# Optimization experiments

Hardware: AMD Instinct MI355X
Metric: run time of the kernel (lower is better)

## Reference

```python
import jax, jax.numpy as jnp
import numpy as np

D_MODEL, D_STATE, D_CONV, EXPAND = 1024, 16, 4, 2
D_INNER = EXPAND * D_MODEL            # 2048
DT_RANK = D_MODEL // 16               # 64
B, L = 2, 4096


def setup_inputs() -> dict:
    key = jax.random.key(0)
    ks = jax.random.split(key, 8)
    s = 0.02
    u = jax.random.normal(ks[0], (B, L, D_MODEL), jnp.float32)
    in_proj_w = jax.random.normal(ks[1], (2 * D_INNER, D_MODEL), jnp.float32) * s
    conv_w = jax.random.normal(ks[2], (D_INNER, D_CONV), jnp.float32) * 0.2
    conv_b = jnp.zeros((D_INNER,), jnp.float32)
    x_proj_w = jax.random.normal(ks[3], (DT_RANK + 2 * D_STATE, D_INNER), jnp.float32) * s
    dt_proj_w = jax.random.normal(ks[4], (D_INNER, DT_RANK), jnp.float32) * (DT_RANK ** -0.5)
    # dt bias initialized so softplus(dt_bias) in [1e-3, 1e-1], as in mamba-ssm
    dt = jnp.exp(jax.random.uniform(ks[5], (D_INNER,)) * (np.log(0.1) - np.log(1e-3)) + np.log(1e-3))
    dt_bias = jnp.log(-jnp.expm1(-dt) * jnp.exp(dt))  # inverse softplus
    A_log = jnp.log(jnp.tile(jnp.arange(1, D_STATE + 1, dtype=jnp.float32), (D_INNER, 1)))
    D_in = jnp.ones((D_INNER,), jnp.float32)
    out_proj_w = jax.random.normal(ks[6], (D_MODEL, D_INNER), jnp.float32) * s
    D_skip = jnp.ones((D_MODEL,), jnp.float32)
    return dict(u=u, in_proj_w=in_proj_w, conv_w=conv_w, conv_b=conv_b,
                x_proj_w=x_proj_w, dt_proj_w=dt_proj_w, dt_bias=dt_bias,
                A_log=A_log, D_in=D_in, out_proj_w=out_proj_w, D_skip=D_skip)


def _mamba(u, in_proj_w, conv_w, conv_b, x_proj_w, dt_proj_w, dt_bias,
           A_log, D_in, out_proj_w):
    b, l, _ = u.shape
    xz = jnp.einsum('bld,ed->ble', u, in_proj_w)      # (B,L,2*Din)
    x, z = jnp.split(xz, 2, axis=-1)
    # causal depthwise conv1d over time, kernel size D_CONV
    xp = jnp.pad(x, ((0, 0), (D_CONV - 1, 0), (0, 0)))
    x = sum(xp[:, k:k + l, :] * conv_w[:, k] for k in range(D_CONV)) + conv_b
    x = jax.nn.silu(x)
    x_dbl = jnp.einsum('bld,ed->ble', x, x_proj_w)    # (B,L,dt_rank+2N)
    dt = jax.nn.softplus(x_dbl[..., :DT_RANK] @ dt_proj_w.T + dt_bias)  # (B,L,Din)
    Bm = x_dbl[..., DT_RANK:DT_RANK + D_STATE]        # (B,L,N)
    Cm = x_dbl[..., DT_RANK + D_STATE:]               # (B,L,N)
    A = -jnp.exp(A_log)                               # (Din,N)

    def step(h, inp):
        dt_t, B_t, C_t, x_t = inp                     # (B,Din),(B,N),(B,N),(B,Din)
        dA = jnp.exp(dt_t[..., None] * A)             # (B,Din,N)
        h = dA * h + (dt_t * x_t)[..., None] * B_t[:, None, :]
        y = jnp.einsum('bdn,bn->bd', h, C_t)
        return h, y

    h0 = jnp.zeros((b, D_INNER, D_STATE), u.dtype)
    xs = (dt.transpose(1, 0, 2), Bm.transpose(1, 0, 2),
          Cm.transpose(1, 0, 2), x.transpose(1, 0, 2))
    _, ys = jax.lax.scan(step, h0, xs)                # (L,B,Din)
    y = ys.transpose(1, 0, 2) + x * D_in
    y = y * jax.nn.silu(z)
    return jnp.einsum('bld,ed->ble', y, out_proj_w)   # (B,L,D_MODEL)


def reference(u, in_proj_w, conv_w, conv_b, x_proj_w, dt_proj_w, dt_bias,
              A_log, D_in, out_proj_w, D_skip):
    y = _mamba(u, in_proj_w, conv_w, conv_b, x_proj_w, dt_proj_w, dt_bias,
               A_log, D_in, out_proj_w)
    return y + D_skip[None, None, :] * u
```

## Files before the change

kernel.cpp:

```cpp
#include <hip/hip_runtime.h>

typedef unsigned short u16;
typedef unsigned int u32;
typedef __attribute__((ext_vector_type(8))) short s16x8;
typedef __attribute__((ext_vector_type(4))) float f32x4;

__device__ inline u16 f2bf(float f){
    u32 u = __float_as_uint(f);
    u32 r = (u + 0x7fffu + ((u >> 16) & 1u)) >> 16;
    return (u16)r;
}
__device__ inline float bf2f(u16 h){
    return __uint_as_float(((u32)h) << 16);
}

#define GLOAD_LDS16(g, l) __builtin_amdgcn_global_load_lds( \
    (__attribute__((address_space(1))) void*)(void*)(g),    \
    (__attribute__((address_space(3))) void*)(l), 16, 0, 0)

#define MEMFENCE asm volatile("" ::: "memory")

template<int EPI>
__global__ __launch_bounds__(512, 1) void gemm256(
    const u16* __restrict__ A, const u16* __restrict__ B,
    int M, int N, int K, int nbn,
    float* __restrict__ Cf, u16* __restrict__ Cb, u16* __restrict__ Cb2,
    const float* __restrict__ aux0, const float* __restrict__ aux1)
{
    __shared__ u16 lds[2][2][2][128 * 64];
    const int tid  = threadIdx.x;
    const int lane = tid & 63, wave = tid >> 6;
    const int wr = wave >> 2, wc = wave & 3;
    const int l16 = lane & 15, lg = lane >> 4;

    int wgid = blockIdx.x, nwg = gridDim.x;
    int swz = wgid;
    if ((nwg & 7) == 0) { int cpx = nwg >> 3; swz = (wgid & 7) * cpx + (wgid >> 3); }
    const int bm = swz / nbn, bn = swz % nbn;

    const u16* Ab = A + (size_t)bm * 256 * K;
    const u16* Bb = B + (size_t)bn * 256 * K;

    auto stage_half = [&](int kbuf, int mat, int half, int kt) {
        const u16* src = mat ? Bb : Ab;
        #pragma unroll
        for (int j = 0; j < 2; j++) {
            int slot = j * 512 + tid;
            int r = slot >> 3, cg = slot & 7;
            GLOAD_LDS16(src + (size_t)(half * 128 + r) * K + kt + ((cg ^ (r & 7)) << 3),
                        &lds[kbuf][mat][half][(j * 512 + wave * 64) * 8]);
        }
    };

    f32x4 acc[2][2][4][2] = {};
    s16x8 a[4][2], b0[2][2], b1[2][2];

    auto readA = [&](int kbuf, int mh) {
        #pragma unroll
        for (int m = 0; m < 4; m++)
            #pragma unroll
            for (int ks = 0; ks < 2; ks++) {
                int r = mh * 64 + m * 16 + l16;
                int cg = (ks * 4 + lg) ^ (l16 & 7);
                a[m][ks] = *(const s16x8*)&lds[kbuf][0][wr][r * 64 + cg * 8];
            }
    };
    auto readB = [&](int kbuf, int nh, s16x8 (&bb)[2][2]) {
        #pragma unroll
        for (int n = 0; n < 2; n++)
            #pragma unroll
            for (int ks = 0; ks < 2; ks++) {
                int row = wc * 64 + nh * 32 + n * 16 + l16;
                int half = row >> 7, r = row & 127;
                int cg = (ks * 4 + lg) ^ (l16 & 7);
                bb[n][ks] = *(const s16x8*)&lds[kbuf][1][half][r * 64 + cg * 8];
            }
    };

    auto phase_mfma = [&](int mh, int nh, s16x8 (&bb)[2][2]) {
        MEMFENCE;
        __builtin_amdgcn_s_barrier();
        asm volatile("s_waitcnt lgkmcnt(0)" ::: "memory");
        __builtin_amdgcn_sched_barrier(0);
        __builtin_amdgcn_s_setprio(1);
        #pragma unroll
        for (int m = 0; m < 4; m++)
            #pragma unroll
            for (int n = 0; n < 2; n++)
                #pragma unroll
                for (int ks = 0; ks < 2; ks++)
                    acc[mh][nh][m][n] = __builtin_amdgcn_mfma_f32_16x16x32_bf16(
                        a[m][ks], bb[n][ks], acc[mh][nh][m][n], 0, 0, 0);
        __builtin_amdgcn_s_setprio(0);
        MEMFENCE;
        __builtin_amdgcn_s_barrier();
        MEMFENCE;
    };

    const int NT = K >> 6;

    stage_half(0, 1, 0, 0); stage_half(0, 1, 1, 0);
    stage_half(0, 0, 0, 0); stage_half(0, 0, 1, 0);
    if (NT > 1) {
        stage_half(1, 1, 0, 64);
        stage_half(1, 0, 0, 64); stage_half(1, 0, 1, 64);
    }
    asm volatile("s_waitcnt vmcnt(6)" ::: "memory");
    MEMFENCE;
    __builtin_amdgcn_s_barrier();
    MEMFENCE;

    for (int it = 0; it < (NT >> 1); it++) {
        const int t1k = (2 * it + 1) << 6;
        const int t2k = (2 * it + 2) << 6;
        const int t3k = (2 * it + 3) << 6;
        const bool pre = (2 * it + 2) < NT;
        readA(0, 0); readB(0, 0, b0);
        stage_half(1, 1, 1, t1k);
        phase_mfma(0, 0, b0);
        readB(0, 1, b1);
        phase_mfma(0, 1, b1);
        readA(0, 1);
        if (pre) stage_half(0, 1, 0, t2k);
        phase_mfma(1, 1, b1);
        if (pre) stage_half(0, 1, 1, t2k);
        asm volatile("s_waitcnt vmcnt(4)" ::: "memory");
        phase_mfma(1, 0, b0);
        readA(1, 0); readB(1, 0, b0);
        if (pre) stage_half(0, 0, 0, t2k);
        phase_mfma(0, 0, b0);
        readB(1, 1, b1);
        if (pre) stage_half(0, 0, 1, t2k);
        phase_mfma(0, 1, b1);
        readA(1, 1);
        if (pre) stage_half(1, 1, 0, t3k);
        phase_mfma(1, 1, b1);
        if (pre) { stage_half(1, 0, 0, t3k); stage_half(1, 0, 1, t3k); }
        asm volatile("s_waitcnt vmcnt(6)" ::: "memory");
        phase_mfma(1, 0, b0);
    }

    #pragma unroll
    for (int mh = 0; mh < 2; mh++)
        #pragma unroll
        for (int nh = 0; nh < 2; nh++)
            #pragma unroll
            for (int m = 0; m < 4; m++)
                #pragma unroll
                for (int n = 0; n < 2; n++) {
                    const int col = bn * 256 + wc * 64 + nh * 32 + n * 16 + l16;
                    #pragma unroll
                    for (int r = 0; r < 4; r++) {
                        const int row = bm * 256 + wr * 128 + mh * 64 + m * 16 + lg * 4 + r;
                        float v = acc[mh][nh][m][n][r];
                        if (EPI == 0) {
                            if (col < 2048) Cb[(size_t)row * 2048 + col] = f2bf(v);
                            else            Cb2[(size_t)row * 2048 + (col - 2048)] = f2bf(v);
                        } else {
                            float o = v + aux0[col] * aux1[(size_t)row * N + col];
                            Cf[(size_t)row * N + col] = o;
                        }
                    }
                }
}

__global__ __launch_bounds__(256) void gemm_dt(
    const u16* __restrict__ A, const u16* __restrict__ B,
    int M, int N, int K,
    u16* __restrict__ Cb, const float* __restrict__ aux0)
{
    constexpr int BK = 64;
    __shared__ u16 As[128 * BK];
    __shared__ u16 Bs[128 * BK];
    const int tid  = threadIdx.x;
    const int lane = tid & 63, wave = tid >> 6;
    const int wr = wave >> 1, wc = wave & 1;
    const int bm = blockIdx.x, bn = blockIdx.y;
    const int l16 = lane & 15, lg = lane >> 4;

    const u16* Ab = A + (size_t)bm * 128 * K;
    const u16* Bb = B + (size_t)bn * 128 * K;

    f32x4 acc[4][4] = {};

    for (int kt = 0; kt < K; kt += BK) {
        #pragma unroll
        for (int p = 0; p < 4; p++) {
            int flat = (p * 256 + tid) * 8;
            int r = flat >> 6, c = flat & 63;
            GLOAD_LDS16(Ab + (size_t)r * K + kt + c, As + flat);
        }
        #pragma unroll
        for (int p = 0; p < 4; p++) {
            int flat = (p * 256 + tid) * 8;
            int r = flat >> 6, c = flat & 63;
            GLOAD_LDS16(Bb + (size_t)r * K + kt + c, Bs + flat);
        }
        asm volatile("s_waitcnt vmcnt(0)" ::: "memory");
        __syncthreads();
        #pragma unroll
        for (int kk = 0; kk < 2; kk++) {
            s16x8 a[4], b[4];
            #pragma unroll
            for (int m = 0; m < 4; m++)
                a[m] = *(const s16x8*)&As[(wr * 64 + m * 16 + l16) * BK + kk * 32 + lg * 8];
            #pragma unroll
            for (int n = 0; n < 4; n++)
                b[n] = *(const s16x8*)&Bs[(wc * 64 + n * 16 + l16) * BK + kk * 32 + lg * 8];
            #pragma unroll
            for (int m = 0; m < 4; m++)
                #pragma unroll
                for (int n = 0; n < 4; n++)
                    acc[m][n] = __builtin_amdgcn_mfma_f32_16x16x32_bf16(a[m], b[n], acc[m][n], 0, 0, 0);
        }
        __syncthreads();
    }

    const int row0 = bm * 128 + wr * 64 + lg * 4;
    const int col0 = bn * 128 + wc * 64 + l16;
    #pragma unroll
    for (int m = 0; m < 4; m++)
        #pragma unroll
        for (int n = 0; n < 4; n++) {
            const int col = col0 + n * 16;
            #pragma unroll
            for (int r = 0; r < 4; r++) {
                const int row = row0 + m * 16 + r;
                float t2 = acc[m][n][r] + aux0[col];
                float sp = (t2 > 15.f) ? t2 : __logf(1.f + __expf(t2));
                Cb[(size_t)row * N + col] = f2bf(sp);
            }
        }
}

__global__ __launch_bounds__(256) void gemm_xproj_sk(
    const u16* __restrict__ A, const u16* __restrict__ B,
    float* __restrict__ part)
{
    constexpr int BK = 64, K = 2048;
    __shared__ u16 As[128 * BK];
    __shared__ u16 Bs[128 * BK];
    const int tid  = threadIdx.x;
    const int lane = tid & 63, wave = tid >> 6;
    const int wr = wave >> 1, wc = wave & 1;
    const int bm = blockIdx.x, sk = blockIdx.y;
    const int l16 = lane & 15, lg = lane >> 4;

    const u16* Ab = A + (size_t)bm * 128 * K;
    const u16* Bb = B;
    const int kt0 = sk * 256;

    f32x4 acc[4][4] = {};

    for (int kt = kt0; kt < kt0 + 256; kt += BK) {
        #pragma unroll
        for (int p = 0; p < 4; p++) {
            int flat = (p * 256 + tid) * 8;
            int r = flat >> 6, c = flat & 63;
            GLOAD_LDS16(Ab + (size_t)r * K + kt + c, As + flat);
        }
        #pragma unroll
        for (int p = 0; p < 4; p++) {
            int flat = (p * 256 + tid) * 8;
            int r = flat >> 6, c = flat & 63;
            GLOAD_LDS16(Bb + (size_t)r * K + kt + c, Bs + flat);
        }
        asm volatile("s_waitcnt vmcnt(0)" ::: "memory");
        __syncthreads();
        #pragma unroll
        for (int kk = 0; kk < 2; kk++) {
            s16x8 a[4], b[4];
            #pragma unroll
            for (int m = 0; m < 4; m++)
                a[m] = *(const s16x8*)&As[(wr * 64 + m * 16 + l16) * BK + kk * 32 + lg * 8];
            #pragma unroll
            for (int n = 0; n < 4; n++)
                b[n] = *(const s16x8*)&Bs[(wc * 64 + n * 16 + l16) * BK + kk * 32 + lg * 8];
            #pragma unroll
            for (int m = 0; m < 4; m++)
                #pragma unroll
                for (int n = 0; n < 4; n++)
                    acc[m][n] = __builtin_amdgcn_mfma_f32_16x16x32_bf16(a[m], b[n], acc[m][n], 0, 0, 0);
        }
        __syncthreads();
    }

    float* pb = part + (size_t)sk * 8192 * 128;
    const int row0 = bm * 128 + wr * 64 + lg * 4;
    const int col0 = wc * 64 + l16;
    #pragma unroll
    for (int m = 0; m < 4; m++)
        #pragma unroll
        for (int n = 0; n < 4; n++)
            #pragma unroll
            for (int r = 0; r < 4; r++)
                pb[(size_t)(row0 + m * 16 + r) * 128 + col0 + n * 16] = acc[m][n][r];
}

__global__ __launch_bounds__(256) void combine_xproj(
    const float* __restrict__ part, u16* __restrict__ dtin,
    float* __restrict__ xBC)
{
    const int gid = blockIdx.x * 256 + threadIdx.x;
    const int row = gid >> 7, col = gid & 127;
    float s = 0.f;
    #pragma unroll
    for (int sk = 0; sk < 8; sk++) s += part[(size_t)sk * 8192 * 128 + gid];
    if (col < 64)      dtin[(size_t)row * 64 + col] = f2bf(s);
    else if (col < 96) xBC[(size_t)row * 32 + (col - 64)] = s;
}

__global__ __launch_bounds__(256) void cvt_all(
    const float* __restrict__ u, const float* __restrict__ Wi,
    const float* __restrict__ Wo, const float* __restrict__ Wdt,
    const float* __restrict__ Wx,
    u16* __restrict__ u_bf, u16* __restrict__ Wi_bf, u16* __restrict__ Wo_bf,
    u16* __restrict__ Wdt_bf, u16* __restrict__ Wx_bf)
{
    size_t i = ((size_t)blockIdx.x * 256 + threadIdx.x) * 4;
    const size_t E0 = 8388608, E1 = E0 + 4194304, E2 = E1 + 2097152, E3 = E2 + 131072;
    f32x4 v;
    u16* dst;
    size_t off;
    if (i < E0)      { off = i;      v = *(const f32x4*)(u + off);   dst = u_bf + off; }
    else if (i < E1) { off = i - E0; v = *(const f32x4*)(Wi + off);  dst = Wi_bf + off; }
    else if (i < E2) { off = i - E1; v = *(const f32x4*)(Wo + off);  dst = Wo_bf + off; }
    else if (i < E3) { off = i - E2; v = *(const f32x4*)(Wdt + off); dst = Wdt_bf + off; }
    else {
        off = i - E3;
        size_t row = off >> 11;
        if (row < 96) v = *(const f32x4*)(Wx + off);
        else          v = (f32x4){0.f, 0.f, 0.f, 0.f};
        dst = Wx_bf + off;
    }
    ushort4 o;
    o.x = f2bf(v[0]); o.y = f2bf(v[1]); o.z = f2bf(v[2]); o.w = f2bf(v[3]);
    *(ushort4*)dst = o;
}

__global__ __launch_bounds__(256) void conv_silu(
    const u16* __restrict__ xzx, const float* __restrict__ cw,
    const float* __restrict__ cb, u16* __restrict__ xc)
{
    const int tid = threadIdx.x;
    const int d0 = tid * 8;
    const int t0 = blockIdx.x * 16;
    const int b  = blockIdx.y;
    float W0[8], W1[8], W2[8], W3[8], BI[8];
    #pragma unroll
    for (int j = 0; j < 8; j++) {
        f32x4 w = *(const f32x4*)(cw + (size_t)(d0 + j) * 4);
        W0[j] = w[0]; W1[j] = w[1]; W2[j] = w[2]; W3[j] = w[3];
        BI[j] = cb[d0 + j];
    }
    const u16* xp = xzx + (size_t)(b * 4096) * 2048 + d0;
    u16* op = xc + (size_t)(b * 4096) * 2048 + d0;

    float x0[8], x1[8], x2[8];
    #pragma unroll
    for (int j = 0; j < 8; j++) { x0[j] = 0.f; x1[j] = 0.f; x2[j] = 0.f; }
    if (t0 >= 3) {
        s16x8 v0 = *(const s16x8*)(xp + (size_t)(t0 - 3) * 2048);
        s16x8 v1 = *(const s16x8*)(xp + (size_t)(t0 - 2) * 2048);
        s16x8 v2 = *(const s16x8*)(xp + (size_t)(t0 - 1) * 2048);
        #pragma unroll
        for (int j = 0; j < 8; j++) {
            x0[j] = bf2f((u16)v0[j]); x1[j] = bf2f((u16)v1[j]); x2[j] = bf2f((u16)v2[j]);
        }
    }
    #pragma unroll
    for (int k = 0; k < 16; k++) {
        int t = t0 + k;
        s16x8 cv = *(const s16x8*)(xp + (size_t)t * 2048);
        s16x8 o;
        #pragma unroll
        for (int j = 0; j < 8; j++) {
            float c = bf2f((u16)cv[j]);
            float s = BI[j] + W0[j] * x0[j] + W1[j] * x1[j] + W2[j] * x2[j] + W3[j] * c;
            float v = s * __fdividef(1.f, 1.f + __expf(-s));
            o[j] = (short)f2bf(v);
            x0[j] = x1[j]; x1[j] = x2[j]; x2[j] = c;
        }
        *(s16x8*)(op + (size_t)t * 2048) = o;
    }
}

__global__ __launch_bounds__(256) void scan_p1(
    const u16* __restrict__ dtb, const u16* __restrict__ xc,
    const float* __restrict__ xBC, const float* __restrict__ A_log,
    u16* __restrict__ Aagg, u16* __restrict__ Bagg)
{
    __shared__ float Bsh[64][16];
    const int tid = threadIdx.x;
    const int d = blockIdx.x * 256 + tid;
    const int c = blockIdx.y, b = blockIdx.z;

    {
        int ti = tid >> 2, p = tid & 3;
        f32x4 bv = *(const f32x4*)(xBC + ((size_t)(b * 4096 + c * 64 + ti)) * 32 + p * 4);
        *(f32x4*)&Bsh[ti][p * 4] = bv;
    }
    __syncthreads();

    float Adn[16];
    #pragma unroll
    for (int q = 0; q < 4; q++) {
        f32x4 al = *(const f32x4*)(A_log + (size_t)d * 16 + q * 4);
        #pragma unroll
        for (int j = 0; j < 4; j++) Adn[q * 4 + j] = -__expf(al[j]);
    }

    const size_t base = (size_t)(b * 4096 + c * 64) * 2048 + d;
    const u16* dtp = dtb + base;
    const u16* xp  = xc  + base;

    float h[16];
    #pragma unroll
    for (int n = 0; n < 16; n++) h[n] = 0.f;
    float sumdt = 0.f;

    float dtv = bf2f(dtp[0]), xv = bf2f(xp[0]);
    for (int t = 0; t < 64; t++) {
        float ndt = 0.f, nx = 0.f;
        if (t < 63) { ndt = bf2f(dtp[(size_t)(t + 1) * 2048]); nx = bf2f(xp[(size_t)(t + 1) * 2048]); }
        float dtx = dtv * xv;
        sumdt += dtv;
        f32x4 B0 = *(const f32x4*)&Bsh[t][0];
        f32x4 B1 = *(const f32x4*)&Bsh[t][4];
        f32x4 B2 = *(const f32x4*)&Bsh[t][8];
        f32x4 B3 = *(const f32x4*)&Bsh[t][12];
        #pragma unroll
        for (int n = 0; n < 16; n++) {
            float Bv = (n < 4) ? B0[n] : (n < 8) ? B1[n - 4] : (n < 12) ? B2[n - 8] : B3[n - 12];
            float aa = __expf(Adn[n] * dtv);
            h[n] = fmaf(aa, h[n], dtx * Bv);
        }
        dtv = ndt; xv = nx;
    }

    const size_t abase = ((size_t)(b * 2048 + d) * 16) * 64 + c;
    #pragma unroll
    for (int n = 0; n < 16; n++) {
        Aagg[abase + (size_t)n * 64] = f2bf(__expf(Adn[n] * sumdt));
        Bagg[abase + (size_t)n * 64] = f2bf(h[n]);
    }
}

__global__ __launch_bounds__(256) void scan_p2(
    const u16* __restrict__ Aagg, u16* __restrict__ BaggH0)
{
    const int gid = blockIdx.x * 256 + threadIdx.x;
    const size_t base = (size_t)gid * 64;
    s16x8 Ar[8], Br[8];
    #pragma unroll
    for (int i = 0; i < 8; i++) {
        Ar[i] = *(const s16x8*)(Aagg + base + i * 8);
        Br[i] = *(const s16x8*)(BaggH0 + base + i * 8);
    }
    s16x8 Hr[8];
    float h = 0.f;
    #pragma unroll
    for (int i = 0; i < 8; i++) {
        #pragma unroll
        for (int j = 0; j < 8; j++) {
            float ac = bf2f((u16)Ar[i][j]);
            float bc = bf2f((u16)Br[i][j]);
            Hr[i][j] = (short)f2bf(h);
            h = fmaf(ac, h, bc);
        }
    }
    #pragma unroll
    for (int i = 0; i < 8; i++)
        *(s16x8*)(BaggH0 + base + i * 8) = Hr[i];
}

__global__ __launch_bounds__(256) void scan_p3(
    const u16* __restrict__ dtb, const u16* __restrict__ xc,
    const float* __restrict__ xBC, const float* __restrict__ A_log,
    const u16* __restrict__ H0, const u16* __restrict__ xzz,
    const float* __restrict__ D_in, u16* __restrict__ yy)
{
    __shared__ float BCs[64][32];
    const int tid = threadIdx.x;
    const int d = blockIdx.x * 256 + tid;
    const int c = blockIdx.y, b = blockIdx.z;

    {
        int ti = tid >> 2, p = tid & 3;
        const float* src = xBC + ((size_t)(b * 4096 + c * 64 + ti)) * 32 + p * 8;
        f32x4 v0 = *(const f32x4*)src;
        f32x4 v1 = *(const f32x4*)(src + 4);
        *(f32x4*)&BCs[ti][p * 8] = v0;
        *(f32x4*)&BCs[ti][p * 8 + 4] = v1;
    }
    __syncthreads();

    float Adn[16];
    #pragma unroll
    for (int q = 0; q < 4; q++) {
        f32x4 al = *(const f32x4*)(A_log + (size_t)d * 16 + q * 4);
        #pragma unroll
        for (int j = 0; j < 4; j++) Adn[q * 4 + j] = -__expf(al[j]);
    }
    const float Dd = D_in[d];

    float h[16];
    const size_t hbase = ((size_t)(b * 2048 + d) * 16) * 64 + c;
    #pragma unroll
    for (int n = 0; n < 16; n++) h[n] = bf2f(H0[hbase + (size_t)n * 64]);

    const size_t base = (size_t)(b * 4096 + c * 64) * 2048 + d;
    const u16* dtp = dtb + base;
    const u16* xp  = xc  + base;
    const u16* zp  = xzz + base;
    u16* yp = yy + base;

    float dtv = bf2f(dtp[0]), xv = bf2f(xp[0]), zv = bf2f(zp[0]);
    for (int t = 0; t < 64; t++) {
        float ndt = 0.f, nx = 0.f, nz = 0.f;
        if (t < 63) {
            ndt = bf2f(dtp[(size_t)(t + 1) * 2048]);
            nx  = bf2f(xp[(size_t)(t + 1) * 2048]);
            nz  = bf2f(zp[(size_t)(t + 1) * 2048]);
        }
        float dtx = dtv * xv;
        f32x4 B0 = *(const f32x4*)&BCs[t][0];
        f32x4 B1 = *(const f32x4*)&BCs[t][4];
        f32x4 B2 = *(const f32x4*)&BCs[t][8];
        f32x4 B3 = *(const f32x4*)&BCs[t][12];
        f32x4 C0 = *(const f32x4*)&BCs[t][16];
        f32x4 C1 = *(const f32x4*)&BCs[t][20];
        f32x4 C2 = *(const f32x4*)&BCs[t][24];
        f32x4 C3 = *(const f32x4*)&BCs[t][28];
        float y = 0.f;
        #pragma unroll
        for (int n = 0; n < 16; n++) {
            float Bv = (n < 4) ? B0[n] : (n < 8) ? B1[n - 4] : (n < 12) ? B2[n - 8] : B3[n - 12];
            float Cv = (n < 4) ? C0[n] : (n < 8) ? C1[n - 4] : (n < 12) ? C2[n - 8] : C3[n - 12];
            float aa = __expf(Adn[n] * dtv);
            h[n] = fmaf(aa, h[n], dtx * Bv);
            y = fmaf(h[n], Cv, y);
        }
        float sz = zv * __fdividef(1.f, 1.f + __expf(-zv));
        float val = fmaf(xv, Dd, y) * sz;
        yp[(size_t)t * 2048] = f2bf(val);
        dtv = ndt; xv = nx; zv = nz;
    }
}

extern "C" void kernel_launch(void* const* d_in, const int* in_sizes, int n_in,
                              void* d_out, int out_size, void* d_ws, size_t ws_size,
                              hipStream_t stream)
{
    const float* u       = (const float*)d_in[0];
    const float* Wi      = (const float*)d_in[1];
    const float* conv_w  = (const float*)d_in[2];
    const float* conv_b  = (const float*)d_in[3];
    const float* Wx      = (const float*)d_in[4];
    const float* Wdt     = (const float*)d_in[5];
    const float* dt_bias = (const float*)d_in[6];
    const float* A_log   = (const float*)d_in[7];
    const float* D_in_   = (const float*)d_in[8];
    const float* Wo      = (const float*)d_in[9];
    const float* D_skip  = (const float*)d_in[10];
    float* out = (float*)d_out;
    (void)in_sizes; (void)n_in; (void)out_size;

    const size_t MB = 1u << 20;
    char* ws = (char*)d_ws;
    u16*   xzx    = (u16*)(ws + 0);
    float* xpart  = (float*)(ws + 0);
    u16*   Aagg   = (u16*)(ws + 0);
    u16*   BaggH0 = (u16*)(ws + 8 * MB);
    u16*   xzz    = (u16*)(ws + 32 * MB);
    u16*   xc     = (u16*)(ws + 64 * MB);
    u16*   u_bf   = (u16*)(ws + 96 * MB);
    u16*   Wi_bf  = (u16*)(ws + 112 * MB);
    u16*   dtb    = (u16*)(ws + 96 * MB);
    u16*   Wx_bf  = (u16*)(ws + 128 * MB);
    u16*   Wdt_bf = (u16*)(ws + 128 * MB + 512 * 1024);
    u16*   yybuf  = (u16*)(ws + 128 * MB);
    float* xBC    = (float*)(ws + 160 * MB);
    u16*   dtin   = (u16*)(ws + 161 * MB);
    u16*   Wo_bf  = (u16*)(ws + 162 * MB);
    const size_t NEED = 166 * MB;
    if (ws_size < NEED) return;

    cvt_all<<<14720, 256, 0, stream>>>(u, Wi, Wo, Wdt, Wx,
                                       u_bf, Wi_bf, Wo_bf, Wdt_bf, Wx_bf);

    gemm256<0><<<512, 512, 0, stream>>>(u_bf, Wi_bf, 8192, 4096, 1024, 16,
                                        nullptr, xzx, xzz, nullptr, nullptr);
    conv_silu<<<dim3(256, 2), 256, 0, stream>>>(xzx, conv_w, conv_b, xc);

    gemm_xproj_sk<<<dim3(64, 8), 256, 0, stream>>>(xc, Wx_bf, xpart);
    combine_xproj<<<4096, 256, 0, stream>>>(xpart, dtin, xBC);

    gemm_dt<<<dim3(64, 16), 256, 0, stream>>>(dtin, Wdt_bf, 8192, 2048, 64,
                                              dtb, dt_bias);

    scan_p1<<<dim3(8, 64, 2), 256, 0, stream>>>(dtb, xc, xBC, A_log, Aagg, BaggH0);
    scan_p2<<<256, 256, 0, stream>>>(Aagg, BaggH0);
    scan_p3<<<dim3(8, 64, 2), 256, 0, stream>>>(dtb, xc, xBC, A_log, BaggH0, xzz,
                                                D_in_, yybuf);

    gemm256<3><<<128, 512, 0, stream>>>(yybuf, Wo_bf, 8192, 1024, 2048, 4,
                                        out, nullptr, nullptr, D_skip, u);
}
```

Before: 383.4 us.

## Double-buffer GEMM fragment registers to overlap LDS reads with MFMA

The GEMM main loop now keeps separate register sets for A and B fragments (AX/AY, BX/BY, B1). The next phase's LDS reads are issued before the current phase's MFMAs, instead of waiting on lgkmcnt(0) before each MFMA block. This is meant to hide LDS read latency behind matrix work across the eight phases per iteration. The cost is higher VGPR pressure, and dropping the explicit waitcnt and sched_barrier leaves ordering to the compiler.

```diff
diff --git a/kernel.cpp b/kernel.cpp
--- a/kernel.cpp
+++ b/kernel.cpp
@@ -19,6 +19,7 @@
     (__attribute__((address_space(3))) void*)(l), 16, 0, 0)
 
 #define MEMFENCE asm volatile("" ::: "memory")
+#define BAR do { MEMFENCE; __builtin_amdgcn_s_barrier(); MEMFENCE; } while (0)
 
 template<int EPI>
 __global__ __launch_bounds__(512, 1) void gemm256(
@@ -53,19 +54,19 @@
     };
 
     f32x4 acc[2][2][4][2] = {};
-    s16x8 a[4][2], b0[2][2], b1[2][2];
-
-    auto readA = [&](int kbuf, int mh) {
+    s16x8 AX[4][2], AY[4][2], BX[2][2], BY[2][2], B1[2][2];
+
+    auto readA = [&](int kbuf, int mh, s16x8 (&dst)[4][2]) {
         #pragma unroll
         for (int m = 0; m < 4; m++)
             #pragma unroll
             for (int ks = 0; ks < 2; ks++) {
                 int r = mh * 64 + m * 16 + l16;
                 int cg = (ks * 4 + lg) ^ (l16 & 7);
-                a[m][ks] = *(const s16x8*)&lds[kbuf][0][wr][r * 64 + cg * 8];
+                dst[m][ks] = *(const s16x8*)&lds[kbuf][0][wr][r * 64 + cg * 8];
             }
     };
-    auto readB = [&](int kbuf, int nh, s16x8 (&bb)[2][2]) {
+    auto readB = [&](int kbuf, int nh, s16x8 (&dst)[2][2]) {
         #pragma unroll
         for (int n = 0; n < 2; n++)
             #pragma unroll
@@ -73,15 +74,10 @@
                 int row = wc * 64 + nh * 32 + n * 16 + l16;
                 int half = row >> 7, r = row & 127;
                 int cg = (ks * 4 + lg) ^ (l16 & 7);
-                bb[n][ks] = *(const s16x8*)&lds[kbuf][1][half][r * 64 + cg * 8];
+                dst[n][ks] = *(const s16x8*)&lds[kbuf][1][half][r * 64 + cg * 8];
             }
     };
-
-    auto phase_mfma = [&](int mh, int nh, s16x8 (&bb)[2][2]) {
-        MEMFENCE;
-        __builtin_amdgcn_s_barrier();
-        asm volatile("s_waitcnt lgkmcnt(0)" ::: "memory");
-        __builtin_amdgcn_sched_barrier(0);
+    auto mfma16 = [&](int mh, int nh, s16x8 (&aa)[4][2], s16x8 (&bb)[2][2]) {
         __builtin_amdgcn_s_setprio(1);
         #pragma unroll
         for (int m = 0; m < 4; m++)
@@ -90,54 +86,51 @@
                 #pragma unroll
                 for (int ks = 0; ks < 2; ks++)
                     acc[mh][nh][m][n] = __builtin_amdgcn_mfma_f32_16x16x32_bf16(
-                        a[m][ks], bb[n][ks], acc[mh][nh][m][n], 0, 0, 0);
+                        aa[m][ks], bb[n][ks], acc[mh][nh][m][n], 0, 0, 0);
         __builtin_amdgcn_s_setprio(0);
-        MEMFENCE;
-        __builtin_amdgcn_s_barrier();
-        MEMFENCE;
     };
 
     const int NT = K >> 6;
 
     stage_half(0, 1, 0, 0); stage_half(0, 1, 1, 0);
     stage_half(0, 0, 0, 0); stage_half(0, 0, 1, 0);
-    if (NT > 1) {
-        stage_half(1, 1, 0, 64);
-        stage_half(1, 0, 0, 64); stage_half(1, 0, 1, 64);
-    }
+    stage_half(1, 1, 0, 64);
+    stage_half(1, 0, 0, 64); stage_half(1, 0, 1, 64);
     asm volatile("s_waitcnt vmcnt(6)" ::: "memory");
-    MEMFENCE;
-    __builtin_amdgcn_s_barrier();
-    MEMFENCE;
+    BAR;
+    readA(0, 0, AX); readB(0, 0, BX);
 
     for (int it = 0; it < (NT >> 1); it++) {
         const int t1k = (2 * it + 1) << 6;
         const int t2k = (2 * it + 2) << 6;
         const int t3k = (2 * it + 3) << 6;
         const bool pre = (2 * it + 2) < NT;
-        readA(0, 0); readB(0, 0, b0);
         stage_half(1, 1, 1, t1k);
-        phase_mfma(0, 0, b0);
-        readB(0, 1, b1);
-        phase_mfma(0, 1, b1);
-        readA(0, 1);
+        BAR; readB(0, 1, B1); mfma16(0, 0, AX, BX); BAR;
+        BAR; readA(0, 1, AY); mfma16(0, 1, AX, B1); BAR;
         if (pre) stage_half(0, 1, 0, t2k);
-        phase_mfma(1, 1, b1);
-        if (pre) stage_half(0, 1, 1, t2k);
-        asm volatile("s_waitcnt vmcnt(4)" ::: "memory");
-        phase_mfma(1, 0, b0);
-        readA(1, 0); readB(1, 0, b0);
+        BAR; mfma16(1, 1, AY, B1); BAR;
+        if (pre) {
+            stage_half(0, 1, 1, t2k);
+            asm volatile("s_waitcnt vmcnt(4)" ::: "memory");
+        } else {
+            asm volatile("s_waitcnt vmcnt(0)" ::: "memory");
+        }
+        BAR; readA(1, 0, AX); readB(1, 0, BY); mfma16(1, 0, AY, BX); BAR;
         if (pre) stage_half(0, 0, 0, t2k);
-        phase_mfma(0, 0, b0);
-        readB(1, 1, b1);
+        BAR; readB(1, 1, B1); mfma16(0, 0, AX, BY); BAR;
         if (pre) stage_half(0, 0, 1, t2k);
-        phase_mfma(0, 1, b1);
-        readA(1, 1);
+        BAR; readA(1, 1, AY); mfma16(0, 1, AX, B1); BAR;
         if (pre) stage_half(1, 1, 0, t3k);
-        phase_mfma(1, 1, b1);
-        if (pre) { stage_half(1, 0, 0, t3k); stage_half(1, 0, 1, t3k); }
-        asm volatile("s_waitcnt vmcnt(6)" ::: "memory");
-        phase_mfma(1, 0, b0);
+        BAR; mfma16(1, 1, AY, B1); BAR;
+        if (pre) {
+            stage_half(1, 0, 0, t3k); stage_half(1, 0, 1, t3k);
+            asm volatile("s_waitcnt vmcnt(6)" ::: "memory");
+        }
+        BAR;
+        if (pre) { readA(0, 0, AX); readB(0, 0, BX); }
+        mfma16(1, 0, AY, BY);
+        BAR;
     }
 
     #pragma unroll
```

New measurement: 536.0 us. 1.4x slower.
